# Optimization experiments

Measured on AMD Instinct MI355X. Metric: run time of the kernel, lower is better.

Reference implementation:

```python
import jax, jax.numpy as jnp
import numpy as np

# Grid configuration (from PointBasedTransformConfig / data dict)
G = 64                      # mast3r grid size per axis
NUM_VOXELS = G * G * G      # 262144
K = 16                      # max_points_in_voxel
RES = 0.02                  # mast3r_grid_resolution
MIN_CORNER = -(G * RES) / 2.0  # cube centered at origin, side G*RES = 1.28
N_POINTS = 2_000_000


def setup_inputs() -> dict:
    key = jax.random.key(0)
    k1, k2, k3, k4 = jax.random.split(key, 4)
    # points uniform in [-0.8, 0.8]^3 so roughly half are inside the 1.28 cube
    pts_0 = (jax.random.uniform(k1, (N_POINTS, 3), dtype=jnp.float32) - 0.5) * 1.6
    conf = jax.random.uniform(k2, (N_POINTS,), dtype=jnp.float32)
    desc = jax.random.normal(k3, (N_POINTS, 24), dtype=jnp.float32)
    desc_conf = jax.random.normal(k4, (N_POINTS,), dtype=jnp.float32)
    return {"pts_0": pts_0, "conf": conf, "desc": desc, "desc_conf": desc_conf}


def _voxelize(pts_0, conf):
    """Returns pts_in_grid: (NUM_VOXELS, K) int32 point indices (or -1)."""
    n = pts_0.shape[0]
    # voxel index per point; out-of-bounds points get sentinel id NUM_VOXELS
    idx = jnp.floor((pts_0 - MIN_CORNER) / RES).astype(jnp.int32)  # (N,3)
    valid = jnp.all((idx >= 0) & (idx < G), axis=-1)               # (N,)
    vox = idx[:, 0] * (G * G) + idx[:, 1] * G + idx[:, 2]
    vox = jnp.where(valid, vox, NUM_VOXELS)
    # stable sort by confidence, descending (jnp.argsort is stable)
    order_conf = jnp.argsort(-conf)                 # point ids, conf-desc order
    vox_c = vox[order_conf]
    # stable sort by voxel id (preserves conf-desc order within each voxel)
    order_vox = jnp.argsort(vox_c)
    vox_s = vox_c[order_vox]                        # sorted voxel ids
    pid_s = order_conf[order_vox]                   # original point ids
    # bincount + exclusive cumsum -> per-voxel offsets -> position within voxel
    counts = jnp.bincount(vox_s, length=NUM_VOXELS + 1)
    offsets = jnp.cumsum(counts) - counts
    pos = jnp.arange(n, dtype=jnp.int32) - offsets[vox_s].astype(jnp.int32)
    # capacity-bounded scatter of point ids into the voxel grid
    ok = (pos < K) & (vox_s < NUM_VOXELS)
    rows = jnp.where(ok, vox_s, NUM_VOXELS)         # dump row for rejects
    cols = jnp.where(ok, pos, 0)
    vals = jnp.where(ok, pid_s, -1).astype(jnp.int32)
    grid = jnp.full((NUM_VOXELS + 1, K), -1, dtype=jnp.int32)
    grid = grid.at[rows, cols].set(vals)
    return grid[:NUM_VOXELS]


def reference(pts_0, conf, desc, desc_conf):
    pts_in_grid = _voxelize(pts_0, conf)            # (V, K) int32
    # gather per-point features into the grid; empty slots -> 0
    feat = jnp.concatenate(
        [pts_0, conf[:, None], desc, desc_conf[:, None]], axis=-1
    )                                               # (N, 29)
    safe = jnp.maximum(pts_in_grid, 0)
    occ = (pts_in_grid >= 0)[..., None].astype(feat.dtype)
    X = feat[safe] * occ                            # (V, K, 29)
    return pts_in_grid, X
```

## Files before the change

### kernel.cpp

```cpp
#include <hip/hip_runtime.h>
#include <limits.h>
#include <math.h>

#define GRID 64
#define NUM_VOXELS (GRID * GRID * GRID)
#define KSLOTS 16
#define CAP 32
#define FEAT 29

typedef float f32x4 __attribute__((ext_vector_type(4)));

__global__ __launch_bounds__(256) void scatter_kernel(
    const float* __restrict__ pts, const float* __restrict__ conf, int n,
    int* __restrict__ cnt, unsigned long long* __restrict__ buf) {
    int i = blockIdx.x * blockDim.x + threadIdx.x;
    if (i >= n) return;
    const float minc = (float)(-(64.0 * 0.02) / 2.0);
    const float rinv = 50.0f;
    float x = pts[(size_t)i * 3 + 0];
    float y = pts[(size_t)i * 3 + 1];
    float z = pts[(size_t)i * 3 + 2];
    int ix = (int)floorf((x - minc) * rinv);
    int iy = (int)floorf((y - minc) * rinv);
    int iz = (int)floorf((z - minc) * rinv);
    if ((unsigned)ix >= GRID || (unsigned)iy >= GRID || (unsigned)iz >= GRID) return;
    int v = ix * (GRID * GRID) + iy * GRID + iz;
    int pos = atomicAdd(&cnt[v], 1);
    if (pos < CAP) {
        unsigned int cb = __float_as_uint(conf[i]);
        unsigned long long key =
            ((unsigned long long)cb << 32) | (unsigned int)(~i);
        buf[(size_t)v * CAP + pos] = key;
    }
}

__global__ __launch_bounds__(256) void select_gather_kernel(
    const float* __restrict__ pts, const float* __restrict__ conf,
    const float* __restrict__ desc, const float* __restrict__ desc_conf,
    const int* __restrict__ cnt, const unsigned long long* __restrict__ buf,
    float* __restrict__ out_idx, float* __restrict__ out_feat) {
    const int tid = threadIdx.x;
    const int vbase = blockIdx.x * 16;

    __shared__ int spid[256];
    __shared__ __align__(16) float st[256 * FEAT];

    if (tid < 16) {
        int v = vbase + tid;
        unsigned long long top[KSLOTS];
        #pragma unroll
        for (int s = 0; s < KSLOTS; ++s) top[s] = 0ULL;
        int n = cnt[v];
        if (n > CAP) n = CAP;
        const unsigned long long* row = buf + (size_t)v * CAP;
        for (int j = 0; j < n; ++j) {
            unsigned long long key = row[j];
            #pragma unroll
            for (int s = 0; s < KSLOTS; ++s) {
                unsigned long long hi = key > top[s] ? key : top[s];
                unsigned long long lo = key > top[s] ? top[s] : key;
                top[s] = hi;
                key    = lo;
            }
        }
        #pragma unroll
        for (int s = 0; s < KSLOTS; ++s) {
            unsigned long long k = top[s];
            spid[tid * 16 + s] = (k != 0ULL) ? (int)(~(unsigned int)k) : -1;
        }
    }
    __syncthreads();

    int pid = spid[tid];
    __builtin_nontemporal_store((float)pid, &out_idx[(size_t)vbase * KSLOTS + tid]);

    float f[FEAT];
    #pragma unroll
    for (int e = 0; e < FEAT; ++e) f[e] = 0.0f;
    if (pid >= 0) {
        f[0] = pts[(size_t)pid * 3 + 0];
        f[1] = pts[(size_t)pid * 3 + 1];
        f[2] = pts[(size_t)pid * 3 + 2];
        f[3] = conf[pid];
        const f32x4* d4 = (const f32x4*)(desc) + (size_t)pid * 6;
        #pragma unroll
        for (int q = 0; q < 6; ++q) {
            f32x4 d = __builtin_nontemporal_load(&d4[q]);
            f[4 + q * 4 + 0] = d.x;
            f[4 + q * 4 + 1] = d.y;
            f[4 + q * 4 + 2] = d.z;
            f[4 + q * 4 + 3] = d.w;
        }
        f[28] = desc_conf[pid];
    }
    #pragma unroll
    for (int e = 0; e < FEAT; ++e) st[tid * FEAT + e] = f[e];
    __syncthreads();

    f32x4* dst = (f32x4*)(out_feat + (size_t)vbase * KSLOTS * FEAT);
    const f32x4* src = (const f32x4*)st;
    #pragma unroll
    for (int k = tid; k < 256 * FEAT / 4; k += 256)
        __builtin_nontemporal_store(src[k], &dst[k]);
}

__global__ __launch_bounds__(256) void select_kernel(
    const int* __restrict__ cnt, const unsigned long long* __restrict__ buf,
    float* __restrict__ out_idx) {
    int v = blockIdx.x * blockDim.x + threadIdx.x;
    if (v >= NUM_VOXELS) return;
    unsigned long long top[KSLOTS];
    #pragma unroll
    for (int s = 0; s < KSLOTS; ++s) top[s] = 0ULL;
    int n = cnt[v];
    if (n > CAP) n = CAP;
    const unsigned long long* row = buf + (size_t)v * CAP;
    for (int j = 0; j < n; ++j) {
        unsigned long long key = row[j];
        #pragma unroll
        for (int s = 0; s < KSLOTS; ++s) {
            unsigned long long hi = key > top[s] ? key : top[s];
            unsigned long long lo = key > top[s] ? top[s] : key;
            top[s] = hi;
            key    = lo;
        }
    }
    float* o = out_idx + (size_t)v * KSLOTS;
    #pragma unroll
    for (int s = 0; s < KSLOTS; ++s) {
        unsigned long long k = top[s];
        o[s] = (float)((k != 0ULL) ? (int)(~(unsigned int)k) : -1);
    }
}

__global__ __launch_bounds__(256) void gather_kernel(
    const float* __restrict__ pts, const float* __restrict__ conf,
    const float* __restrict__ desc, const float* __restrict__ desc_conf,
    const float* __restrict__ out_idx, float* __restrict__ out_feat) {
    const int t = threadIdx.x;
    const size_t slot0 = (size_t)blockIdx.x * 256;
    const size_t slot  = slot0 + t;
    __shared__ __align__(16) float st[256 * FEAT];
    int pid = (int)out_idx[slot];
    float f[FEAT];
    #pragma unroll
    for (int e = 0; e < FEAT; ++e) f[e] = 0.0f;
    if (pid >= 0) {
        f[0] = pts[(size_t)pid * 3 + 0];
        f[1] = pts[(size_t)pid * 3 + 1];
        f[2] = pts[(size_t)pid * 3 + 2];
        f[3] = conf[pid];
        const f32x4* d4 = (const f32x4*)(desc) + (size_t)pid * 6;
        #pragma unroll
        for (int q = 0; q < 6; ++q) {
            f32x4 d = d4[q];
            f[4 + q * 4 + 0] = d.x; f[4 + q * 4 + 1] = d.y;
            f[4 + q * 4 + 2] = d.z; f[4 + q * 4 + 3] = d.w;
        }
        f[28] = desc_conf[pid];
    }
    #pragma unroll
    for (int e = 0; e < FEAT; ++e) st[t * FEAT + e] = f[e];
    __syncthreads();
    f32x4* dst = (f32x4*)(out_feat + slot0 * FEAT);
    const f32x4* src = (const f32x4*)st;
    #pragma unroll
    for (int k = t; k < 256 * FEAT / 4; k += 256) dst[k] = src[k];
}

extern "C" void kernel_launch(void* const* d_in, const int* in_sizes, int n_in,
                              void* d_out, int out_size, void* d_ws, size_t ws_size,
                              hipStream_t stream) {
    const float* pts       = (const float*)d_in[0];
    const float* conf      = (const float*)d_in[1];
    const float* desc      = (const float*)d_in[2];
    const float* desc_conf = (const float*)d_in[3];
    const int n = in_sizes[1];

    float* out_idx  = (float*)d_out;
    float* out_feat = out_idx + (size_t)NUM_VOXELS * KSLOTS;

    const size_t need = (size_t)NUM_VOXELS * 4
                      + (size_t)NUM_VOXELS * CAP * 8;

    if (ws_size >= need) {
        int* cnt = (int*)d_ws;
        unsigned long long* buf = (unsigned long long*)((char*)d_ws + (size_t)NUM_VOXELS * 4);
        (void)hipMemsetAsync(cnt, 0, NUM_VOXELS * sizeof(int), stream);
        scatter_kernel<<<(n + 255) / 256, 256, 0, stream>>>(pts, conf, n, cnt, buf);
        select_gather_kernel<<<NUM_VOXELS / 16, 256, 0, stream>>>(
            pts, conf, desc, desc_conf, cnt, buf, out_idx, out_feat);
    } else {
        int* cnt = (int*)out_feat;
        unsigned long long* buf = (unsigned long long*)(out_feat + NUM_VOXELS);
        (void)hipMemsetAsync(cnt, 0, NUM_VOXELS * sizeof(int), stream);
        scatter_kernel<<<(n + 255) / 256, 256, 0, stream>>>(pts, conf, n, cnt, buf);
        select_kernel<<<NUM_VOXELS / 256, 256, 0, stream>>>(cnt, buf, out_idx);
        gather_kernel<<<(NUM_VOXELS * KSLOTS) / 256, 256, 0, stream>>>(
            pts, conf, desc, desc_conf, out_idx, out_feat);
    }
}
```

Measured before the change: 280.3 us.

## Split fused select-gather into full-parallel select and gather kernels with staged conf

Replaces the fused select+gather kernel, where only 16 of 256 threads performed the top-K selection, with a select kernel that runs one thread per voxel followed by a separate gather kernel. The select kernel also writes each slot's confidence, taken from the sort key, into a staging buffer so the gather reads it contiguously instead of doing a random conf lookup. This removes the serialized selection phase and its low thread utilization, at the cost of an extra launch, an extra workspace buffer, and a round trip of the indices through global memory. The fallback path now also uses nontemporal stores.

```diff
diff --git a/kernel.cpp b/kernel.cpp
--- a/kernel.cpp
+++ b/kernel.cpp
@@ -34,79 +34,9 @@
     }
 }
 
-__global__ __launch_bounds__(256) void select_gather_kernel(
-    const float* __restrict__ pts, const float* __restrict__ conf,
-    const float* __restrict__ desc, const float* __restrict__ desc_conf,
-    const int* __restrict__ cnt, const unsigned long long* __restrict__ buf,
-    float* __restrict__ out_idx, float* __restrict__ out_feat) {
-    const int tid = threadIdx.x;
-    const int vbase = blockIdx.x * 16;
-
-    __shared__ int spid[256];
-    __shared__ __align__(16) float st[256 * FEAT];
-
-    if (tid < 16) {
-        int v = vbase + tid;
-        unsigned long long top[KSLOTS];
-        #pragma unroll
-        for (int s = 0; s < KSLOTS; ++s) top[s] = 0ULL;
-        int n = cnt[v];
-        if (n > CAP) n = CAP;
-        const unsigned long long* row = buf + (size_t)v * CAP;
-        for (int j = 0; j < n; ++j) {
-            unsigned long long key = row[j];
-            #pragma unroll
-            for (int s = 0; s < KSLOTS; ++s) {
-                unsigned long long hi = key > top[s] ? key : top[s];
-                unsigned long long lo = key > top[s] ? top[s] : key;
-                top[s] = hi;
-                key    = lo;
-            }
-        }
-        #pragma unroll
-        for (int s = 0; s < KSLOTS; ++s) {
-            unsigned long long k = top[s];
-            spid[tid * 16 + s] = (k != 0ULL) ? (int)(~(unsigned int)k) : -1;
-        }
-    }
-    __syncthreads();
-
-    int pid = spid[tid];
-    __builtin_nontemporal_store((float)pid, &out_idx[(size_t)vbase * KSLOTS + tid]);
-
-    float f[FEAT];
-    #pragma unroll
-    for (int e = 0; e < FEAT; ++e) f[e] = 0.0f;
-    if (pid >= 0) {
-        f[0] = pts[(size_t)pid * 3 + 0];
-        f[1] = pts[(size_t)pid * 3 + 1];
-        f[2] = pts[(size_t)pid * 3 + 2];
-        f[3] = conf[pid];
-        const f32x4* d4 = (const f32x4*)(desc) + (size_t)pid * 6;
-        #pragma unroll
-        for (int q = 0; q < 6; ++q) {
-            f32x4 d = __builtin_nontemporal_load(&d4[q]);
-            f[4 + q * 4 + 0] = d.x;
-            f[4 + q * 4 + 1] = d.y;
-            f[4 + q * 4 + 2] = d.z;
-            f[4 + q * 4 + 3] = d.w;
-        }
-        f[28] = desc_conf[pid];
-    }
-    #pragma unroll
-    for (int e = 0; e < FEAT; ++e) st[tid * FEAT + e] = f[e];
-    __syncthreads();
-
-    f32x4* dst = (f32x4*)(out_feat + (size_t)vbase * KSLOTS * FEAT);
-    const f32x4* src = (const f32x4*)st;
-    #pragma unroll
-    for (int k = tid; k < 256 * FEAT / 4; k += 256)
-        __builtin_nontemporal_store(src[k], &dst[k]);
-}
-
 __global__ __launch_bounds__(256) void select_kernel(
     const int* __restrict__ cnt, const unsigned long long* __restrict__ buf,
-    float* __restrict__ out_idx) {
+    float* __restrict__ out_idx, float* __restrict__ stagedC) {
     int v = blockIdx.x * blockDim.x + threadIdx.x;
     if (v >= NUM_VOXELS) return;
     unsigned long long top[KSLOTS];
@@ -126,14 +56,81 @@
         }
     }
     float* o = out_idx + (size_t)v * KSLOTS;
+    float* c = stagedC + (size_t)v * KSLOTS;
     #pragma unroll
     for (int s = 0; s < KSLOTS; ++s) {
         unsigned long long k = top[s];
         o[s] = (float)((k != 0ULL) ? (int)(~(unsigned int)k) : -1);
+        c[s] = __uint_as_float((unsigned int)(k >> 32));
     }
 }
 
 __global__ __launch_bounds__(256) void gather_kernel(
+    const float* __restrict__ pts, const float* __restrict__ stagedC,
+    const float* __restrict__ desc, const float* __restrict__ desc_conf,
+    const float* __restrict__ out_idx, float* __restrict__ out_feat) {
+    const int t = threadIdx.x;
+    const size_t slot0 = (size_t)blockIdx.x * 256;
+    const size_t slot  = slot0 + t;
+    __shared__ __align__(16) float st[256 * FEAT];
+    int pid = (int)out_idx[slot];
+    float f[FEAT];
+    #pragma unroll
+    for (int e = 0; e < FEAT; ++e) f[e] = 0.0f;
+    if (pid >= 0) {
+        f[0] = pts[(size_t)pid * 3 + 0];
+        f[1] = pts[(size_t)pid * 3 + 1];
+        f[2] = pts[(size_t)pid * 3 + 2];
+        f[3] = stagedC[slot];
+        const f32x4* d4 = (const f32x4*)(desc) + (size_t)pid * 6;
+        #pragma unroll
+        for (int q = 0; q < 6; ++q) {
+            f32x4 d = d4[q];
+            f[4 + q * 4 + 0] = d.x; f[4 + q * 4 + 1] = d.y;
+            f[4 + q * 4 + 2] = d.z; f[4 + q * 4 + 3] = d.w;
+        }
+        f[28] = desc_conf[pid];
+    }
+    #pragma unroll
+    for (int e = 0; e < FEAT; ++e) st[t * FEAT + e] = f[e];
+    __syncthreads();
+    f32x4* dst = (f32x4*)(out_feat + slot0 * FEAT);
+    const f32x4* src = (const f32x4*)st;
+    #pragma unroll
+    for (int k = t; k < 256 * FEAT / 4; k += 256)
+        __builtin_nontemporal_store(src[k], &dst[k]);
+}
+
+__global__ __launch_bounds__(256) void select_kernel_nf(
+    const int* __restrict__ cnt, const unsigned long long* __restrict__ buf,
+    float* __restrict__ out_idx) {
+    int v = blockIdx.x * blockDim.x + threadIdx.x;
+    if (v >= NUM_VOXELS) return;
+    unsigned long long top[KSLOTS];
+    #pragma unroll
+    for (int s = 0; s < KSLOTS; ++s) top[s] = 0ULL;
+    int n = cnt[v];
+    if (n > CAP) n = CAP;
+    const unsigned long long* row = buf + (size_t)v * CAP;
+    for (int j = 0; j < n; ++j) {
+        unsigned long long key = row[j];
+        #pragma unroll
+        for (int s = 0; s < KSLOTS; ++s) {
+            unsigned long long hi = key > top[s] ? key : top[s];
+            unsigned long long lo = key > top[s] ? top[s] : key;
+            top[s] = hi;
+            key    = lo;
+        }
+    }
+    float* o = out_idx + (size_t)v * KSLOTS;
+    #pragma unroll
+    for (int s = 0; s < KSLOTS; ++s) {
+        unsigned long long k = top[s];
+        o[s] = (float)((k != 0ULL) ? (int)(~(unsigned int)k) : -1);
+    }
+}
+
+__global__ __launch_bounds__(256) void gather_kernel_nf(
     const float* __restrict__ pts, const float* __restrict__ conf,
     const float* __restrict__ desc, const float* __restrict__ desc_conf,
     const float* __restrict__ out_idx, float* __restrict__ out_feat) {
@@ -165,7 +162,8 @@
     f32x4* dst = (f32x4*)(out_feat + slot0 * FEAT);
     const f32x4* src = (const f32x4*)st;
     #pragma unroll
-    for (int k = t; k < 256 * FEAT / 4; k += 256) dst[k] = src[k];
+    for (int k = t; k < 256 * FEAT / 4; k += 256)
+        __builtin_nontemporal_store(src[k], &dst[k]);
 }
 
 extern "C" void kernel_launch(void* const* d_in, const int* in_sizes, int n_in,
@@ -180,23 +178,26 @@
     float* out_idx  = (float*)d_out;
     float* out_feat = out_idx + (size_t)NUM_VOXELS * KSLOTS;
 
-    const size_t need = (size_t)NUM_VOXELS * 4
-                      + (size_t)NUM_VOXELS * CAP * 8;
-
-    if (ws_size >= need) {
+    const size_t sz_cnt  = (size_t)NUM_VOXELS * 4;
+    const size_t sz_buf  = (size_t)NUM_VOXELS * CAP * 8;
+    const size_t sz_stgc = (size_t)NUM_VOXELS * KSLOTS * 4;
+
+    if (ws_size >= sz_cnt + sz_buf + sz_stgc) {
         int* cnt = (int*)d_ws;
-        unsigned long long* buf = (unsigned long long*)((char*)d_ws + (size_t)NUM_VOXELS * 4);
-        (void)hipMemsetAsync(cnt, 0, NUM_VOXELS * sizeof(int), stream);
+        unsigned long long* buf = (unsigned long long*)((char*)d_ws + sz_cnt);
+        float* stagedC = (float*)((char*)d_ws + sz_cnt + sz_buf);
+        (void)hipMemsetAsync(cnt, 0, sz_cnt, stream);
         scatter_kernel<<<(n + 255) / 256, 256, 0, stream>>>(pts, conf, n, cnt, buf);
-        select_gather_kernel<<<NUM_VOXELS / 16, 256, 0, stream>>>(
-            pts, conf, desc, desc_conf, cnt, buf, out_idx, out_feat);
+        select_kernel<<<NUM_VOXELS / 256, 256, 0, stream>>>(cnt, buf, out_idx, stagedC);
+        gather_kernel<<<(NUM_VOXELS * KSLOTS) / 256, 256, 0, stream>>>(
+            pts, stagedC, desc, desc_conf, out_idx, out_feat);
     } else {
         int* cnt = (int*)out_feat;
         unsigned long long* buf = (unsigned long long*)(out_feat + NUM_VOXELS);
-        (void)hipMemsetAsync(cnt, 0, NUM_VOXELS * sizeof(int), stream);
+        (void)hipMemsetAsync(cnt, 0, sz_cnt, stream);
         scatter_kernel<<<(n + 255) / 256, 256, 0, stream>>>(pts, conf, n, cnt, buf);
-        select_kernel<<<NUM_VOXELS / 256, 256, 0, stream>>>(cnt, buf, out_idx);
-        gather_kernel<<<(NUM_VOXELS * KSLOTS) / 256, 256, 0, stream>>>(
+        select_kernel_nf<<<NUM_VOXELS / 256, 256, 0, stream>>>(cnt, buf, out_idx);
+        gather_kernel_nf<<<(NUM_VOXELS * KSLOTS) / 256, 256, 0, stream>>>(
             pts, conf, desc, desc_conf, out_idx, out_feat);
     }
 }
```

Result: faster. 226.7 us, median of 2 (-19.1%).
